# Optimization experiments

Measured on AMD Instinct MI355X. Metric: run time of the kernel, lower is better.

The kernel has to match this reference:

```python
import jax, jax.numpy as jnp
import numpy as np


def setup_inputs() -> dict:
    key = jax.random.key(0)
    k_x, k_w, k_W, k_b, k_idx = jax.random.split(key, 5)
    B, T, D, E, K = 8, 512, 1024, 64, 2
    x = jax.random.normal(k_x, (B, T, D), dtype=jnp.float32)
    w = jax.random.uniform(k_w, (B, K), dtype=jnp.float32)
    # stacked expert banks (kaiming-uniform-like scale)
    bound_W = (6.0 / D) ** 0.5 / (1 + 5.0) ** 0.5
    W_bank = jax.random.uniform(k_W, (E, D, D), minval=-bound_W, maxval=bound_W, dtype=jnp.float32)
    bound_b = 1.0 / D ** 0.5
    b_bank = jax.random.uniform(k_b, (E, D), minval=-bound_b, maxval=bound_b, dtype=jnp.float32)
    idx = jax.random.randint(k_idx, (B, K), 0, E, dtype=jnp.int64)
    return {"x": x, "w": w, "W_bank": W_bank, "b_bank": b_bank, "idx": idx}


def reference(x, w, W_bank, b_bank, idx):
    # x: (B,T,D); w: (B,k); idx: (B,k) int; W_bank: (E,D,D); b_bank: (E,D)
    W_sel = W_bank[idx]           # (B,k,D,D) gather per-token-group expert weights
    b_sel = b_bank[idx]           # (B,k,D)
    # y = act(x @ W[e] + b[e]) per selected expert, note contraction over input dim i
    y_k = jnp.einsum('bti,bkio->btko', x, W_sel) + b_sel[:, None, :, :]
    y_k = jax.nn.relu(y_k)
    y = jnp.sum(y_k * w[:, None, :, None], axis=2)  # weighted combine over k -> (B,T,D)
    return y
```

## Files before the change

kernel.cpp:

```cpp
#include <hip/hip_runtime.h>
#include <stdint.h>

typedef unsigned short ushort_t;
typedef __attribute__((ext_vector_type(8))) short short8;
typedef __attribute__((ext_vector_type(4))) float f32x4;
typedef __attribute__((ext_vector_type(4))) uint32_t u32x4;
typedef __attribute__((ext_vector_type(2))) uint32_t u32x2;

#define B_SZ 8
#define T_SZ 512
#define D_SZ 1024
#define KSTEPS 16

__device__ __forceinline__ ushort_t f2bf(float f) {
  union { float f; uint32_t i; } c; c.f = f;
  uint32_t u = c.i;
  u += 0x7fffu + ((u >> 16) & 1u);
  return (ushort_t)(u >> 16);
}

__device__ __forceinline__ uint32_t pk_bf16(float a, float b) {
#if __has_builtin(__builtin_amdgcn_cvt_pk_bf16_f32)
  typedef __bf16 bf2_t __attribute__((ext_vector_type(2)));
  union { bf2_t v; uint32_t u; } c;
  c.v = __builtin_amdgcn_cvt_pk_bf16_f32(a, b);
  return c.u;
#else
  return (uint32_t)f2bf(a) | ((uint32_t)f2bf(b) << 16);
#endif
}

__global__ __launch_bounds__(512, 2)
void moe_gemm(const float* __restrict__ x, const float* __restrict__ w,
              const float* __restrict__ Wb, const float* __restrict__ bb,
              const int* __restrict__ idx, float* __restrict__ out)
{
  __shared__ union {
    struct { ushort_t A[8192]; ushort_t BT[2][8192]; } st;
    float comb[128 * 128];
  } sm;

  const int tid  = threadIdx.x;
  const int lane = tid & 63;
  const int wave = tid >> 6;
  const int grp  = wave >> 2;
  const int wl   = wave & 3;

  const int bid = blockIdx.x;
  const int b   = bid >> 5;
  const int mt  = (bid >> 3) & 3;
  const int nt  = bid & 7;

  const int   e  = idx[b * 2 + grp];
  const float wk = w[b * 2 + grp];
  const float* Wg = Wb + (size_t)e * (D_SZ * (size_t)D_SZ);

  ushort_t* As = sm.st.A;
  ushort_t* BT = sm.st.BT[grp];

  const int tl = tid & 255;
  const int kg = tl >> 4;
  const int ng = tl & 15;
  const float* Wrow = Wg + (size_t)(kg * 4) * D_SZ + (nt * 128 + ng * 8);

  const int f0 = tid, f1 = 512 + tid;
  const int am0 = f0 >> 3, am1 = f1 >> 3;
  const int kb0 = f0 & 7,  kb1 = f1 & 7;
  const float* xr0 = x + (size_t)(b * T_SZ + mt * 128 + am0) * D_SZ + kb0 * 8;
  const float* xr1 = x + (size_t)(b * T_SZ + mt * 128 + am1) * D_SZ + kb1 * 8;
  ushort_t* ad0 = As + am0 * 64 + (kb0 ^ (am0 & 7)) * 8;
  ushort_t* ad1 = As + am1 * 64 + (kb1 ^ (am1 & 7)) * 8;

  f32x4 wreg[8];
  f32x4 areg[4];
#pragma unroll
  for (int r = 0; r < 4; ++r) {
    wreg[r * 2 + 0] = *(const f32x4*)(Wrow + (size_t)r * D_SZ);
    wreg[r * 2 + 1] = *(const f32x4*)(Wrow + (size_t)r * D_SZ + 4);
  }
  areg[0] = *(const f32x4*)(xr0);
  areg[1] = *(const f32x4*)(xr0 + 4);
  areg[2] = *(const f32x4*)(xr1);
  areg[3] = *(const f32x4*)(xr1 + 4);

  f32x4 acc[4][4];
#pragma unroll
  for (int mi = 0; mi < 4; ++mi)
#pragma unroll
    for (int ni = 0; ni < 4; ++ni) acc[mi][ni] = (f32x4){0.f, 0.f, 0.f, 0.f};

  const int mb = (wl >> 1) * 64;
  const int nb = (wl & 1) * 64;
  const int fm = lane & 15;
  const int quad = lane >> 4;

  for (int step = 0; step < KSTEPS; ++step) {
    {
      u32x4 av0 = { pk_bf16(areg[0][0], areg[0][1]), pk_bf16(areg[0][2], areg[0][3]),
                    pk_bf16(areg[1][0], areg[1][1]), pk_bf16(areg[1][2], areg[1][3]) };
      *(u32x4*)ad0 = av0;
      u32x4 av1 = { pk_bf16(areg[2][0], areg[2][1]), pk_bf16(areg[2][2], areg[2][3]),
                    pk_bf16(areg[3][0], areg[3][1]), pk_bf16(areg[3][2], areg[3][3]) };
      *(u32x4*)ad1 = av1;
#pragma unroll
      for (int j = 0; j < 8; ++j) {
        const int n = ng * 8 + j;
        const int s = (n ^ (n >> 3)) & 7;
        const int elem = n * 64 + (((kg >> 1) ^ s) << 3) + ((kg & 1) << 2);
        const int hi = j >> 2, lo = j & 3;
        u32x2 dv = { pk_bf16(wreg[0 + hi][lo], wreg[2 + hi][lo]),
                     pk_bf16(wreg[4 + hi][lo], wreg[6 + hi][lo]) };
        *(u32x2*)(BT + elem) = dv;
      }
    }
    __syncthreads();

    if (step + 1 < KSTEPS) {
      const float* p = Wrow + (size_t)(step + 1) * 64 * D_SZ;
#pragma unroll
      for (int r = 0; r < 4; ++r) {
        wreg[r * 2 + 0] = *(const f32x4*)(p + (size_t)r * D_SZ);
        wreg[r * 2 + 1] = *(const f32x4*)(p + (size_t)r * D_SZ + 4);
      }
      const int ko = (step + 1) * 64;
      areg[0] = *(const f32x4*)(xr0 + ko);
      areg[1] = *(const f32x4*)(xr0 + ko + 4);
      areg[2] = *(const f32x4*)(xr1 + ko);
      areg[3] = *(const f32x4*)(xr1 + ko + 4);
    }

#pragma unroll
    for (int h = 0; h < 2; ++h) {
      short8 af[4], bfr[4];
#pragma unroll
      for (int mi = 0; mi < 4; ++mi) {
        const int m = mb + mi * 16 + fm;
        const int kbs = (h * 4 + quad) ^ (m & 7);
        af[mi] = *(const short8*)(As + m * 64 + kbs * 8);
      }
#pragma unroll
      for (int ni = 0; ni < 4; ++ni) {
        const int n = nb + ni * 16 + fm;
        const int kbs = (h * 4 + quad) ^ ((n ^ (n >> 3)) & 7);
        bfr[ni] = *(const short8*)(BT + n * 64 + kbs * 8);
      }
#pragma unroll
      for (int mi = 0; mi < 4; ++mi)
#pragma unroll
        for (int ni = 0; ni < 4; ++ni)
          acc[mi][ni] = __builtin_amdgcn_mfma_f32_16x16x32_bf16(af[mi], bfr[ni],
                                                                acc[mi][ni], 0, 0, 0);
    }
    __syncthreads();
  }

  float bias_v[4];
#pragma unroll
  for (int ni = 0; ni < 4; ++ni)
    bias_v[ni] = bb[e * D_SZ + nt * 128 + nb + ni * 16 + fm];

#pragma unroll
  for (int mi = 0; mi < 4; ++mi)
#pragma unroll
    for (int ni = 0; ni < 4; ++ni)
#pragma unroll
      for (int rg = 0; rg < 4; ++rg) {
        float v = acc[mi][ni][rg] + bias_v[ni];
        v = v > 0.f ? v : 0.f;
        acc[mi][ni][rg] = v * wk;
      }

  float* comb = sm.comb;
  if (grp == 1) {
#pragma unroll
    for (int mi = 0; mi < 4; ++mi)
#pragma unroll
      for (int ni = 0; ni < 4; ++ni)
#pragma unroll
        for (int rg = 0; rg < 4; ++rg) {
          const int row = mb + mi * 16 + quad * 4 + rg;
          const int col = nb + ni * 16 + fm;
          comb[row * 128 + col] = acc[mi][ni][rg];
        }
  }
  __syncthreads();
  if (grp == 0) {
#pragma unroll
    for (int mi = 0; mi < 4; ++mi)
#pragma unroll
      for (int ni = 0; ni < 4; ++ni)
#pragma unroll
        for (int rg = 0; rg < 4; ++rg) {
          const int row = mb + mi * 16 + quad * 4 + rg;
          const int col = nb + ni * 16 + fm;
          comb[row * 128 + col] += acc[mi][ni][rg];
        }
  }
  __syncthreads();
#pragma unroll
  for (int r = 0; r < 8; ++r) {
    const int c   = r * 512 + tid;
    const int row = c >> 5;
    const int c4  = c & 31;
    f32x4 v = *(const f32x4*)(comb + row * 128 + c4 * 4);
    *(f32x4*)(out + (size_t)(b * T_SZ + mt * 128 + row) * D_SZ + nt * 128 + c4 * 4) = v;
  }
}

extern "C" void kernel_launch(void* const* d_in, const int* in_sizes, int n_in,
                              void* d_out, int out_size, void* d_ws, size_t ws_size,
                              hipStream_t stream) {
  const float* x  = (const float*)d_in[0];
  const float* w  = (const float*)d_in[1];
  const float* Wb = (const float*)d_in[2];
  const float* bb = (const float*)d_in[3];
  const int*   idx = (const int*)d_in[4];
  float* out = (float*)d_out;
  (void)in_sizes; (void)n_in; (void)out_size; (void)d_ws; (void)ws_size;

  dim3 grid(B_SZ * 4 * 8);
  dim3 block(512);
  hipLaunchKernelGGL(moe_gemm, grid, block, 0, stream, x, w, Wb, bb, idx, out);
}
```

Baseline: 352.7 us.

## Retile MoE GEMM to 256x64 blocks with double-buffered LDS and batch-interleaved grid

Block tile changes from 128x128 to 256x64, so each wave now covers 64 rows by the full 64 columns. Shared-memory A/B buffers are double-buffered, which removes the trailing barrier in each K step. The block index now puts batch in the low bits, so concurrently running blocks touch different experts and x rows, with the aim of spreading HBM traffic and improving L2 reuse of weight columns. The combine buffer uses a padded stride of 68 to avoid LDS bank conflicts. The trade-off is more x loads per block (256 rows) and less reuse of weights per loaded tile.

```diff
diff --git a/kernel.cpp b/kernel.cpp
--- a/kernel.cpp
+++ b/kernel.cpp
@@ -10,7 +10,11 @@
 #define B_SZ 8
 #define T_SZ 512
 #define D_SZ 1024
+#define MT 256
+#define NT 64
+#define BK 64
 #define KSTEPS 16
+#define CSTRIDE 68
 
 __device__ __forceinline__ ushort_t f2bf(float f) {
   union { float f; uint32_t i; } c; c.f = f;
@@ -36,8 +40,11 @@
               const int* __restrict__ idx, float* __restrict__ out)
 {
   __shared__ union {
-    struct { ushort_t A[8192]; ushort_t BT[2][8192]; } st;
-    float comb[128 * 128];
+    struct {
+      ushort_t A[2][MT * BK];
+      ushort_t BT[2][2][NT * BK];
+    } st;
+    float comb[MT * CSTRIDE];
   } sm;
 
   const int tid  = threadIdx.x;
@@ -47,41 +54,40 @@
   const int wl   = wave & 3;
 
   const int bid = blockIdx.x;
-  const int b   = bid >> 5;
-  const int mt  = (bid >> 3) & 3;
-  const int nt  = bid & 7;
+  const int b   = bid & 7;
+  const int rr  = bid >> 3;
+  const int mt  = rr >> 4;
+  const int nt  = rr & 15;
 
   const int   e  = idx[b * 2 + grp];
   const float wk = w[b * 2 + grp];
   const float* Wg = Wb + (size_t)e * (D_SZ * (size_t)D_SZ);
 
-  ushort_t* As = sm.st.A;
-  ushort_t* BT = sm.st.BT[grp];
-
   const int tl = tid & 255;
   const int kg = tl >> 4;
   const int ng = tl & 15;
-  const float* Wrow = Wg + (size_t)(kg * 4) * D_SZ + (nt * 128 + ng * 8);
-
-  const int f0 = tid, f1 = 512 + tid;
-  const int am0 = f0 >> 3, am1 = f1 >> 3;
-  const int kb0 = f0 & 7,  kb1 = f1 & 7;
-  const float* xr0 = x + (size_t)(b * T_SZ + mt * 128 + am0) * D_SZ + kb0 * 8;
-  const float* xr1 = x + (size_t)(b * T_SZ + mt * 128 + am1) * D_SZ + kb1 * 8;
-  ushort_t* ad0 = As + am0 * 64 + (kb0 ^ (am0 & 7)) * 8;
-  ushort_t* ad1 = As + am1 * 64 + (kb1 ^ (am1 & 7)) * 8;
-
-  f32x4 wreg[8];
-  f32x4 areg[4];
-#pragma unroll
-  for (int r = 0; r < 4; ++r) {
-    wreg[r * 2 + 0] = *(const f32x4*)(Wrow + (size_t)r * D_SZ);
-    wreg[r * 2 + 1] = *(const f32x4*)(Wrow + (size_t)r * D_SZ + 4);
-  }
-  areg[0] = *(const f32x4*)(xr0);
-  areg[1] = *(const f32x4*)(xr0 + 4);
-  areg[2] = *(const f32x4*)(xr1);
-  areg[3] = *(const f32x4*)(xr1 + 4);
+  const float* Wrow = Wg + (size_t)(kg * 4) * D_SZ + (nt * NT + ng * 4);
+
+  const float* xr[4];
+  int aoff[4];
+#pragma unroll
+  for (int i = 0; i < 4; ++i) {
+    const int f  = tid + 512 * i;
+    const int am = f >> 3;
+    const int kb = f & 7;
+    xr[i]   = x + (size_t)(b * T_SZ + mt * MT + am) * D_SZ + kb * 8;
+    aoff[i] = am * BK + (kb ^ (am & 7)) * 8;
+  }
+
+  f32x4 areg[8], wreg[4];
+#pragma unroll
+  for (int i = 0; i < 4; ++i) {
+    areg[2 * i + 0] = *(const f32x4*)(xr[i]);
+    areg[2 * i + 1] = *(const f32x4*)(xr[i] + 4);
+  }
+#pragma unroll
+  for (int r = 0; r < 4; ++r)
+    wreg[r] = *(const f32x4*)(Wrow + (size_t)r * D_SZ);
 
   f32x4 acc[4][4];
 #pragma unroll
@@ -89,44 +95,45 @@
 #pragma unroll
     for (int ni = 0; ni < 4; ++ni) acc[mi][ni] = (f32x4){0.f, 0.f, 0.f, 0.f};
 
-  const int mb = (wl >> 1) * 64;
-  const int nb = (wl & 1) * 64;
-  const int fm = lane & 15;
+  const int fm   = lane & 15;
   const int quad = lane >> 4;
+  const int mb   = wl * 64;
 
   for (int step = 0; step < KSTEPS; ++step) {
-    {
-      u32x4 av0 = { pk_bf16(areg[0][0], areg[0][1]), pk_bf16(areg[0][2], areg[0][3]),
-                    pk_bf16(areg[1][0], areg[1][1]), pk_bf16(areg[1][2], areg[1][3]) };
-      *(u32x4*)ad0 = av0;
-      u32x4 av1 = { pk_bf16(areg[2][0], areg[2][1]), pk_bf16(areg[2][2], areg[2][3]),
-                    pk_bf16(areg[3][0], areg[3][1]), pk_bf16(areg[3][2], areg[3][3]) };
-      *(u32x4*)ad1 = av1;
-#pragma unroll
-      for (int j = 0; j < 8; ++j) {
-        const int n = ng * 8 + j;
-        const int s = (n ^ (n >> 3)) & 7;
-        const int elem = n * 64 + (((kg >> 1) ^ s) << 3) + ((kg & 1) << 2);
-        const int hi = j >> 2, lo = j & 3;
-        u32x2 dv = { pk_bf16(wreg[0 + hi][lo], wreg[2 + hi][lo]),
-                     pk_bf16(wreg[4 + hi][lo], wreg[6 + hi][lo]) };
-        *(u32x2*)(BT + elem) = dv;
-      }
+    const int buf = step & 1;
+    ushort_t* As = sm.st.A[buf];
+    ushort_t* Bt = sm.st.BT[buf][grp];
+
+#pragma unroll
+    for (int i = 0; i < 4; ++i) {
+      u32x4 av = { pk_bf16(areg[2*i][0],   areg[2*i][1]),
+                   pk_bf16(areg[2*i][2],   areg[2*i][3]),
+                   pk_bf16(areg[2*i+1][0], areg[2*i+1][1]),
+                   pk_bf16(areg[2*i+1][2], areg[2*i+1][3]) };
+      *(u32x4*)(As + aoff[i]) = av;
+    }
+#pragma unroll
+    for (int j = 0; j < 4; ++j) {
+      const int n = ng * 4 + j;
+      const int s = (n ^ (n >> 3)) & 7;
+      const int elem = n * BK + (((kg >> 1) ^ s) << 3) + ((kg & 1) << 2);
+      u32x2 dv = { pk_bf16(wreg[0][j], wreg[1][j]),
+                   pk_bf16(wreg[2][j], wreg[3][j]) };
+      *(u32x2*)(Bt + elem) = dv;
     }
     __syncthreads();
 
     if (step + 1 < KSTEPS) {
-      const float* p = Wrow + (size_t)(step + 1) * 64 * D_SZ;
-#pragma unroll
-      for (int r = 0; r < 4; ++r) {
-        wreg[r * 2 + 0] = *(const f32x4*)(p + (size_t)r * D_SZ);
-        wreg[r * 2 + 1] = *(const f32x4*)(p + (size_t)r * D_SZ + 4);
-      }
-      const int ko = (step + 1) * 64;
-      areg[0] = *(const f32x4*)(xr0 + ko);
-      areg[1] = *(const f32x4*)(xr0 + ko + 4);
-      areg[2] = *(const f32x4*)(xr1 + ko);
-      areg[3] = *(const f32x4*)(xr1 + ko + 4);
+      const int ko = (step + 1) * BK;
+#pragma unroll
+      for (int i = 0; i < 4; ++i) {
+        areg[2 * i + 0] = *(const f32x4*)(xr[i] + ko);
+        areg[2 * i + 1] = *(const f32x4*)(xr[i] + ko + 4);
+      }
+      const float* p = Wrow + (size_t)ko * D_SZ;
+#pragma unroll
+      for (int r = 0; r < 4; ++r)
+        wreg[r] = *(const f32x4*)(p + (size_t)r * D_SZ);
     }
 
 #pragma unroll
@@ -136,13 +143,13 @@
       for (int mi = 0; mi < 4; ++mi) {
         const int m = mb + mi * 16 + fm;
         const int kbs = (h * 4 + quad) ^ (m & 7);
-        af[mi] = *(const short8*)(As + m * 64 + kbs * 8);
+        af[mi] = *(const short8*)(As + m * BK + kbs * 8);
       }
 #pragma unroll
       for (int ni = 0; ni < 4; ++ni) {
-        const int n = nb + ni * 16 + fm;
+        const int n = ni * 16 + fm;
         const int kbs = (h * 4 + quad) ^ ((n ^ (n >> 3)) & 7);
-        bfr[ni] = *(const short8*)(BT + n * 64 + kbs * 8);
+        bfr[ni] = *(const short8*)(Bt + n * BK + kbs * 8);
       }
 #pragma unroll
       for (int mi = 0; mi < 4; ++mi)
@@ -151,13 +158,12 @@
           acc[mi][ni] = __builtin_amdgcn_mfma_f32_16x16x32_bf16(af[mi], bfr[ni],
                                                                 acc[mi][ni], 0, 0, 0);
     }
-    __syncthreads();
   }
 
   float bias_v[4];
 #pragma unroll
   for (int ni = 0; ni < 4; ++ni)
-    bias_v[ni] = bb[e * D_SZ + nt * 128 + nb + ni * 16 + fm];
+    bias_v[ni] = bb[e * D_SZ + nt * NT + ni * 16 + fm];
 
 #pragma unroll
   for (int mi = 0; mi < 4; ++mi)
@@ -170,6 +176,7 @@
         acc[mi][ni][rg] = v * wk;
       }
 
+  __syncthreads();
   float* comb = sm.comb;
   if (grp == 1) {
 #pragma unroll
@@ -179,8 +186,8 @@
 #pragma unroll
         for (int rg = 0; rg < 4; ++rg) {
           const int row = mb + mi * 16 + quad * 4 + rg;
-          const int col = nb + ni * 16 + fm;
-          comb[row * 128 + col] = acc[mi][ni][rg];
+          const int col = ni * 16 + fm;
+          comb[row * CSTRIDE + col] = acc[mi][ni][rg];
         }
   }
   __syncthreads();
@@ -192,18 +199,19 @@
 #pragma unroll
         for (int rg = 0; rg < 4; ++rg) {
           const int row = mb + mi * 16 + quad * 4 + rg;
-          const int col = nb + ni * 16 + fm;
-          comb[row * 128 + col] += acc[mi][ni][rg];
+          const int col = ni * 16 + fm;
+          comb[row * CSTRIDE + col] += acc[mi][ni][rg];
         }
   }
   __syncthreads();
+
 #pragma unroll
   for (int r = 0; r < 8; ++r) {
     const int c   = r * 512 + tid;
-    const int row = c >> 5;
-    const int c4  = c & 31;
-    f32x4 v = *(const f32x4*)(comb + row * 128 + c4 * 4);
-    *(f32x4*)(out + (size_t)(b * T_SZ + mt * 128 + row) * D_SZ + nt * 128 + c4 * 4) = v;
+    const int row = c >> 4;
+    const int c4  = c & 15;
+    f32x4 v = *(const f32x4*)(comb + row * CSTRIDE + c4 * 4);
+    *(f32x4*)(out + (size_t)(b * T_SZ + mt * MT + row) * D_SZ + nt * NT + c4 * 4) = v;
   }
 }
 
@@ -218,7 +226,7 @@
   float* out = (float*)d_out;
   (void)in_sizes; (void)n_in; (void)out_size; (void)d_ws; (void)ws_size;
 
-  dim3 grid(B_SZ * 4 * 8);
+  dim3 grid(256);
   dim3 block(512);
   hipLaunchKernelGGL(moe_gemm, grid, block, 0, stream, x, w, Wb, bb, idx, out);
 }
```

Result: no change. 347.7 us (-1.4%).
